# Kernel optimization log

Measured on AMD Instinct MI355X. Metric: run time of the kernel, lower is better.

## Reference

```python
import jax, jax.numpy as jnp
import numpy as np

H = 1024   # hidden size
NH = 16    # num attention heads
HD = H // NH  # head dim = 64


def setup_inputs() -> dict:
    key = jax.random.key(0)
    ks = jax.random.split(key, 8)
    B, S = 2, 2048
    scale = 0.02
    return {
        "hidden_states": jax.random.normal(ks[0], (B, S, H), dtype=jnp.float32),
        "attention_mask": jnp.zeros((B, 1, 1, S), dtype=jnp.float32),
        "Wq": jax.random.normal(ks[1], (H, H), dtype=jnp.float32) * scale,
        "bq": jnp.zeros((H,), dtype=jnp.float32),
        "Wk": jax.random.normal(ks[2], (H, H), dtype=jnp.float32) * scale,
        "bk": jnp.zeros((H,), dtype=jnp.float32),
        "Wv": jax.random.normal(ks[3], (H, H), dtype=jnp.float32) * scale,
        "bv": jnp.zeros((H,), dtype=jnp.float32),
    }


def reference(hidden_states, attention_mask, Wq, bq, Wk, bk, Wv, bv):
    B, S, _ = hidden_states.shape

    def split_heads(x):  # [B,S,H] -> [B,NH,S,HD]
        return x.reshape(B, S, NH, HD).transpose(0, 2, 1, 3)

    q = split_heads(hidden_states @ Wq.T + bq)
    k = split_heads(hidden_states @ Wk.T + bk)
    v = split_heads(hidden_states @ Wv.T + bv)

    # raw attention scores [B,NH,S,S]
    scores = jnp.einsum("bhqd,bhkd->bhqk", q, k) / jnp.sqrt(jnp.float32(HD))
    scores = scores + attention_mask  # additive mask, broadcast [B,1,1,S]
    probs = jax.nn.softmax(scores, axis=-1)
    # dropout(p=0.1) is identity in eval mode

    ctx = jnp.einsum("bhqk,bhkd->bhqd", probs, v)  # [B,NH,S,HD]
    return ctx.transpose(0, 2, 1, 3).reshape(B, S, H)
```

## Files before the change

### kernel.cpp

```cpp
#include <hip/hip_runtime.h>
#include <hip/hip_bf16.h>
#include <math.h>

#define HSZ 1024
#define NHD 16
#define SEQ 2048
#define BSZ 2
#define MTOT (BSZ*SEQ)

typedef __attribute__((ext_vector_type(4)))  float  f32x4;
typedef __attribute__((ext_vector_type(8)))  __bf16 bf16x8;

#define LOG2E 1.4426950408889634f

#if __has_builtin(__builtin_amdgcn_exp2f)
#define EXP2(x) __builtin_amdgcn_exp2f(x)
#else
#define EXP2(x) exp2f(x)
#endif

__device__ __forceinline__ unsigned short f2bf(float x) {
    union { float f; unsigned u; } v; v.f = x;
    unsigned r = v.u + 0x7FFFu + ((v.u >> 16) & 1u);
    return (unsigned short)(r >> 16);
}
__device__ __forceinline__ float bf2f(unsigned short u) {
    union { unsigned u; float f; } v; v.u = ((unsigned)u) << 16; return v.f;
}
__device__ __forceinline__ unsigned cvtpk(float lo, float hi) {
    unsigned r;
    asm("v_cvt_pk_bf16_f32 %0, %1, %2" : "=v"(r) : "v"(lo), "v"(hi));
    return r;
}

__global__ __launch_bounds__(256) void cvt_all(
    const float* __restrict__ h,  unsigned short* __restrict__ hd,
    const float* __restrict__ w0, unsigned short* __restrict__ w0d,
    const float* __restrict__ w1, unsigned short* __restrict__ w1d,
    const float* __restrict__ w2, unsigned short* __restrict__ w2d,
    const float* __restrict__ mask, unsigned short* __restrict__ mexpb)
{
    const int bid = blockIdx.x;
    if (bid >= 3584) {
        const int o = ((bid - 3584) * 256 + threadIdx.x) * 8;
        float4 a = *(const float4*)(mask + o);
        float4 b = *(const float4*)(mask + o + 4);
        uint4 v;
        v.x = f2bf(EXP2(a.x * LOG2E)) | ((unsigned)f2bf(EXP2(a.y * LOG2E)) << 16);
        v.y = f2bf(EXP2(a.z * LOG2E)) | ((unsigned)f2bf(EXP2(a.w * LOG2E)) << 16);
        v.z = f2bf(EXP2(b.x * LOG2E)) | ((unsigned)f2bf(EXP2(b.y * LOG2E)) << 16);
        v.w = f2bf(EXP2(b.z * LOG2E)) | ((unsigned)f2bf(EXP2(b.w * LOG2E)) << 16);
        *(uint4*)(mexpb + o) = v;
        return;
    }
    const float* s; unsigned short* d; int i;
    if (bid < 2048)      { s = h;  d = hd;  i = bid; }
    else if (bid < 2560) { s = w0; d = w0d; i = bid - 2048; }
    else if (bid < 3072) { s = w1; d = w1d; i = bid - 2560; }
    else                 { s = w2; d = w2d; i = bid - 3072; }
    const int o = (i * 256 + threadIdx.x) * 8;
    float4 a = *(const float4*)(s + o);
    float4 b = *(const float4*)(s + o + 4);
    uint4 v;
    v.x = f2bf(a.x) | ((unsigned)f2bf(a.y) << 16);
    v.y = f2bf(a.z) | ((unsigned)f2bf(a.w) << 16);
    v.z = f2bf(b.x) | ((unsigned)f2bf(b.y) << 16);
    v.w = f2bf(b.z) | ((unsigned)f2bf(b.w) << 16);
    *(uint4*)(d + o) = v;
}

__global__ __launch_bounds__(256) void qkv_gemm(
    const unsigned short* __restrict__ hb,
    const unsigned short* __restrict__ wq,
    const unsigned short* __restrict__ wk,
    const unsigned short* __restrict__ wv,
    const float* __restrict__ bq, const float* __restrict__ bk,
    const float* __restrict__ bv, const unsigned short* __restrict__ mexpb,
    unsigned short* __restrict__ qo, char* __restrict__ ko,
    char* __restrict__ vo)
{
    __shared__ __align__(16) unsigned short As[128 * 32];
    __shared__ __align__(16) unsigned short Bs[128 * 32];

    const int t = threadIdx.x;
    const int w = t >> 6, l = t & 63, g = l >> 4, c = l & 15;
    const int bn = blockIdx.x, bm = blockIdx.y;
    const int which = bn >> 3;
    const int n0 = (bn & 7) << 7;
    const int m0 = bm << 7;
    const unsigned short* W = (which == 0) ? wq : (which == 1) ? wk : wv;
    const float* bb = (which == 0) ? bq : (which == 1) ? bk : bv;
    const float scale = (which == 0) ? 0.125f * LOG2E : 1.0f;
    const int wr = w >> 1, wc = w & 1;

    float mexpf[16];
    if (which == 2) {
        #pragma unroll
        for (int mi = 0; mi < 4; ++mi) {
            const int mrow = m0 + wr * 64 + mi * 16 + g * 4;
            const int bi = mrow >> 11, si = mrow & 2047;
            const unsigned short* mp = mexpb + bi * SEQ + si;
            uint2 mv = *(const uint2*)mp;
            mexpf[mi * 4 + 0] = bf2f((unsigned short)(mv.x & 0xFFFF));
            mexpf[mi * 4 + 1] = bf2f((unsigned short)(mv.x >> 16));
            mexpf[mi * 4 + 2] = bf2f((unsigned short)(mv.y & 0xFFFF));
            mexpf[mi * 4 + 3] = bf2f((unsigned short)(mv.y >> 16));
        }
    }

    f32x4 acc[4][4];
    #pragma unroll
    for (int mi = 0; mi < 4; ++mi)
        #pragma unroll
        for (int ni = 0; ni < 4; ++ni) acc[mi][ni] = {0.f, 0.f, 0.f, 0.f};

    for (int k0 = 0; k0 < HSZ; k0 += 32) {
        #pragma unroll
        for (int i2 = 0; i2 < 2; ++i2) {
            const int chunk = 2 * w + i2;
            const int row = (chunk << 4) + (l >> 2);
            const int sg = (l & 3) ^ ((row >> 1) & 3);
            const char* ga = (const char*)hb +
                (((size_t)(m0 + row) << 10) + k0) * 2 + sg * 16;
            const char* gb = (const char*)W +
                (((size_t)(n0 + row) << 10) + k0) * 2 + sg * 16;
            __builtin_amdgcn_global_load_lds(
                (const __attribute__((address_space(1))) unsigned*)ga,
                (__attribute__((address_space(3))) unsigned*)((char*)As + chunk * 1024),
                16, 0, 0);
            __builtin_amdgcn_global_load_lds(
                (const __attribute__((address_space(1))) unsigned*)gb,
                (__attribute__((address_space(3))) unsigned*)((char*)Bs + chunk * 1024),
                16, 0, 0);
        }
        __syncthreads();

        bf16x8 af[4], bfr[4];
        #pragma unroll
        for (int mi = 0; mi < 4; ++mi) {
            const int row = wr * 64 + mi * 16 + c;
            const int gg = g ^ ((row >> 1) & 3);
            af[mi] = *(const bf16x8*)((const char*)As + row * 64 + gg * 16);
        }
        #pragma unroll
        for (int ni = 0; ni < 4; ++ni) {
            const int row = wc * 64 + ni * 16 + c;
            const int gg = g ^ ((row >> 1) & 3);
            bfr[ni] = *(const bf16x8*)((const char*)Bs + row * 64 + gg * 16);
        }
        #pragma unroll
        for (int mi = 0; mi < 4; ++mi)
            #pragma unroll
            for (int ni = 0; ni < 4; ++ni)
                acc[mi][ni] = __builtin_amdgcn_mfma_f32_16x16x32_bf16(
                    af[mi], bfr[ni], acc[mi][ni], 0, 0, 0);
        __syncthreads();
    }

    #pragma unroll
    for (int ni = 0; ni < 4; ++ni) {
        const int ncol = n0 + wc * 64 + ni * 16 + c;
        const int hh = ncol >> 6, d = ncol & 63;
        const float bsc = bb[ncol] * scale;
        #pragma unroll
        for (int mi = 0; mi < 4; ++mi) {
            #pragma unroll
            for (int j = 0; j < 4; ++j) {
                const int mrow = m0 + wr * 64 + mi * 16 + g * 4 + j;
                const int bi = mrow >> 11, si = mrow & 2047;
                float vf = acc[mi][ni][j] * scale + bsc;
                if (which == 2) vf *= mexpf[mi * 4 + j];
                const unsigned short val = f2bf(vf);
                const size_t bhoff = (size_t)(bi * NHD + hh);
                if (which == 0) {
                    qo[((bhoff * SEQ + si) << 6) + d] = val;
                } else if (which == 1) {
                    char* p = ko + (bhoff << 18) + ((size_t)(si >> 6) << 13)
                            + ((si & 63) << 7) + (((d << 1)) ^ ((si & 7) << 4));
                    *(unsigned short*)p = val;
                } else {
                    char* p = vo + (bhoff << 18) + ((size_t)(si >> 6) << 13)
                            + (d << 7) + (((si & 63) << 1) ^ ((d & 7) << 4));
                    *(unsigned short*)p = val;
                }
            }
        }
    }
}

__global__ __launch_bounds__(256) void attn_mfma(
    const unsigned short* __restrict__ qb, const char* __restrict__ kb,
    const char* __restrict__ vb, const unsigned short* __restrict__ mexpb,
    float* __restrict__ out)
{
    __shared__ __align__(16) char Kt[3][8192];
    __shared__ __align__(16) char Vt[3][8192];
    __shared__ __align__(16) unsigned Pl[4][16][32];

    const int t = threadIdx.x;
    const int w = t >> 6, l = t & 63, g = l >> 4, c = l & 15;
    const int qt = blockIdx.x, h = blockIdx.y, b = blockIdx.z;
    const int bh = b * NHD + h;
    const int q0 = qt * 128 + w * 32;

    const unsigned short* qp = qb + ((size_t)bh * SEQ + q0) * 64;
    const char* kbase = kb + ((size_t)bh << 18);
    const char* vbase = vb + ((size_t)bh << 18);
    const unsigned short* mep = mexpb + b * SEQ;

    bf16x8 qf[2][2];
    #pragma unroll
    for (int qh = 0; qh < 2; ++qh)
        #pragma unroll
        for (int p = 0; p < 2; ++p)
            qf[qh][p] = *(const bf16x8*)(qp + (qh * 16 + c) * 64 + p * 32 + g * 8);

    f32x4 o0[4], o1[4];
    #pragma unroll
    for (int tt = 0; tt < 4; ++tt) { o0[tt] = {0.f,0.f,0.f,0.f}; o1[tt] = {0.f,0.f,0.f,0.f}; }
    f32x4 ls0 = {0.f,0.f,0.f,0.f}, ls1 = {0.f,0.f,0.f,0.f};

    auto STAGE = [&](int tile, int buf) {
        const char* kg = kbase + tile * 8192 + w * 2048 + l * 16;
        const char* vg = vbase + tile * 8192 + w * 2048 + l * 16;
        #pragma unroll
        for (int i = 0; i < 2; ++i) {
            __builtin_amdgcn_global_load_lds(
                (const __attribute__((address_space(1))) unsigned*)(kg + i * 1024),
                (__attribute__((address_space(3))) unsigned*)(&Kt[buf][w * 2048 + i * 1024]),
                16, 0, 0);
            __builtin_amdgcn_global_load_lds(
                (const __attribute__((address_space(1))) unsigned*)(vg + i * 1024),
                (__attribute__((address_space(3))) unsigned*)(&Vt[buf][w * 2048 + i * 1024]),
                16, 0, 0);
        }
    };

    STAGE(0, 0);
    STAGE(1, 1);

    int cur = 0;
    for (int kt = 0; kt < 32; ++kt) {
        const int kv0 = kt * 64;

        if (kt >= 30) { asm volatile("s_waitcnt vmcnt(0)" ::: "memory"); }
        else          { asm volatile("s_waitcnt vmcnt(4)" ::: "memory"); }
        __builtin_amdgcn_s_barrier();
        __builtin_amdgcn_sched_barrier(0);

        if (kt < 30) {
            int slot = cur + 2; if (slot >= 3) slot -= 3;
            STAGE(kt + 2, slot);
        }

        bf16x8 mf[2];
        #pragma unroll
        for (int blk = 0; blk < 2; ++blk)
            mf[blk] = *(const bf16x8*)(mep + kv0 + blk * 32 + g * 8);

        f32x4 s0[4], s1[4];
        #pragma unroll
        for (int t2 = 0; t2 < 4; ++t2) { s0[t2] = {0.f,0.f,0.f,0.f}; s1[t2] = {0.f,0.f,0.f,0.f}; }
        __builtin_amdgcn_s_setprio(1);
        #pragma unroll
        for (int t2 = 0; t2 < 4; ++t2) {
            const bf16x8 k0 = *(const bf16x8*)(&Kt[cur][(t2 * 16 + c) * 128
                                 + ((g * 16) ^ ((c & 7) << 4))]);
            const bf16x8 k1 = *(const bf16x8*)(&Kt[cur][(t2 * 16 + c) * 128
                                 + ((64 + g * 16) ^ ((c & 7) << 4))]);
            s0[t2] = __builtin_amdgcn_mfma_f32_16x16x32_bf16(k0, qf[0][0], s0[t2], 0, 0, 0);
            s0[t2] = __builtin_amdgcn_mfma_f32_16x16x32_bf16(k1, qf[0][1], s0[t2], 0, 0, 0);
            s1[t2] = __builtin_amdgcn_mfma_f32_16x16x32_bf16(k0, qf[1][0], s1[t2], 0, 0, 0);
            s1[t2] = __builtin_amdgcn_mfma_f32_16x16x32_bf16(k1, qf[1][1], s1[t2], 0, 0, 0);
        }
        __builtin_amdgcn_s_setprio(0);

        bf16x8 vfr[4][2];
        #pragma unroll
        for (int tt = 0; tt < 4; ++tt)
            #pragma unroll
            for (int blk = 0; blk < 2; ++blk)
                vfr[tt][blk] = *(const bf16x8*)(&Vt[cur][(tt * 16 + c) * 128
                                     + ((blk * 64 + g * 16) ^ ((c & 7) << 4))]);

        #pragma unroll
        for (int t2 = 0; t2 < 4; ++t2) {
            s0[t2][0] = EXP2(s0[t2][0]); s0[t2][1] = EXP2(s0[t2][1]);
            s0[t2][2] = EXP2(s0[t2][2]); s0[t2][3] = EXP2(s0[t2][3]);
        }
        #pragma unroll
        for (int t2 = 0; t2 < 4; ++t2) {
            uint2 pr;
            pr.x = cvtpk(s0[t2][0], s0[t2][1]);
            pr.y = cvtpk(s0[t2][2], s0[t2][3]);
            *(uint2*)&Pl[w][c][(8 * t2 + 2 * g) ^ ((c & 7) << 2)] = pr;
        }
        {
            bf16x8 pfr[2];
            #pragma unroll
            for (int blk = 0; blk < 2; ++blk)
                pfr[blk] = *(const bf16x8*)&Pl[w][c][(16 * blk + 4 * g) ^ ((c & 7) << 2)];
            __builtin_amdgcn_s_setprio(1);
            #pragma unroll
            for (int blk = 0; blk < 2; ++blk)
                ls0 = __builtin_amdgcn_mfma_f32_16x16x32_bf16(mf[blk], pfr[blk], ls0, 0, 0, 0);
            #pragma unroll
            for (int tt = 0; tt < 4; ++tt)
                #pragma unroll
                for (int blk = 0; blk < 2; ++blk)
                    o0[tt] = __builtin_amdgcn_mfma_f32_16x16x32_bf16(vfr[tt][blk], pfr[blk], o0[tt], 0, 0, 0);
            __builtin_amdgcn_s_setprio(0);
        }

        #pragma unroll
        for (int t2 = 0; t2 < 4; ++t2) {
            s1[t2][0] = EXP2(s1[t2][0]); s1[t2][1] = EXP2(s1[t2][1]);
            s1[t2][2] = EXP2(s1[t2][2]); s1[t2][3] = EXP2(s1[t2][3]);
        }
        #pragma unroll
        for (int t2 = 0; t2 < 4; ++t2) {
            uint2 pr;
            pr.x = cvtpk(s1[t2][0], s1[t2][1]);
            pr.y = cvtpk(s1[t2][2], s1[t2][3]);
            *(uint2*)&Pl[w][c][(8 * t2 + 2 * g) ^ ((c & 7) << 2)] = pr;
        }
        {
            bf16x8 pfr[2];
            #pragma unroll
            for (int blk = 0; blk < 2; ++blk)
                pfr[blk] = *(const bf16x8*)&Pl[w][c][(16 * blk + 4 * g) ^ ((c & 7) << 2)];
            __builtin_amdgcn_s_setprio(1);
            #pragma unroll
            for (int blk = 0; blk < 2; ++blk)
                ls1 = __builtin_amdgcn_mfma_f32_16x16x32_bf16(mf[blk], pfr[blk], ls1, 0, 0, 0);
            #pragma unroll
            for (int tt = 0; tt < 4; ++tt)
                #pragma unroll
                for (int blk = 0; blk < 2; ++blk)
                    o1[tt] = __builtin_amdgcn_mfma_f32_16x16x32_bf16(vfr[tt][blk], pfr[blk], o1[tt], 0, 0, 0);
            __builtin_amdgcn_s_setprio(0);
        }

        ++cur; if (cur == 3) cur = 0;
    }

    const float li0 = 1.f / ls0[0];
    const float li1 = 1.f / ls1[0];
    #pragma unroll
    for (int tt = 0; tt < 4; ++tt) {
        const size_t r0 = ((size_t)(b * SEQ + q0 + c) << 10) + h * 64 + 16 * tt + 4 * g;
        out[r0 + 0] = o0[tt][0] * li0;
        out[r0 + 1] = o0[tt][1] * li0;
        out[r0 + 2] = o0[tt][2] * li0;
        out[r0 + 3] = o0[tt][3] * li0;
        const size_t r1 = ((size_t)(b * SEQ + q0 + 16 + c) << 10) + h * 64 + 16 * tt + 4 * g;
        out[r1 + 0] = o1[tt][0] * li1;
        out[r1 + 1] = o1[tt][1] * li1;
        out[r1 + 2] = o1[tt][2] * li1;
        out[r1 + 3] = o1[tt][3] * li1;
    }
}

extern "C" void kernel_launch(void* const* d_in, const int* in_sizes, int n_in,
                              void* d_out, int out_size, void* d_ws, size_t ws_size,
                              hipStream_t stream) {
    const float* hid  = (const float*)d_in[0];
    const float* mask = (const float*)d_in[1];
    const float* Wq   = (const float*)d_in[2];
    const float* bq   = (const float*)d_in[3];
    const float* Wk   = (const float*)d_in[4];
    const float* bk   = (const float*)d_in[5];
    const float* Wv   = (const float*)d_in[6];
    const float* bv   = (const float*)d_in[7];
    float* out = (float*)d_out;

    char* ws = (char*)d_ws;
    unsigned short* qbf = (unsigned short*)(ws);
    char*           kbf = ws + 8388608;
    char*           vbf = ws + 16777216;
    unsigned short* hbf = (unsigned short*)(ws + 25165824);
    unsigned short* wqb = (unsigned short*)(ws + 33554432);
    unsigned short* wkb = (unsigned short*)(ws + 35651584);
    unsigned short* wvb = (unsigned short*)(ws + 37748736);
    unsigned short* mxb = (unsigned short*)(ws + 39845888);

    cvt_all<<<3586, 256, 0, stream>>>(hid, hbf, Wq, wqb, Wk, wkb, Wv, wvb,
                                      mask, mxb);
    qkv_gemm<<<dim3(24, 32), 256, 0, stream>>>(hbf, wqb, wkb, wvb,
                                               bq, bk, bv, mxb, qbf, kbf, vbf);
    attn_mfma<<<dim3(16, NHD, BSZ), 256, 0, stream>>>(qbf, kbf, vbf, mxb, out);
}
```

Measured before the change: 115.6 us.

## Triple-buffer QKV GEMM LDS tiles with async prefetch two stages ahead

The QKV projection GEMM's shared-memory tiles become a three-slot ring buffer. Global-to-LDS loads for k-step kk+2 are issued before the MFMA work of step kk, with explicit vmcnt waits and a single barrier per iteration replacing the two __syncthreads. MFMA issue priority is also raised with s_setprio. This is meant to hide global load latency in the GEMM, at the cost of three times the LDS footprint, which may lower occupancy.

```diff
diff --git a/kernel.cpp b/kernel.cpp
--- a/kernel.cpp
+++ b/kernel.cpp
@@ -79,8 +79,8 @@
     unsigned short* __restrict__ qo, char* __restrict__ ko,
     char* __restrict__ vo)
 {
-    __shared__ __align__(16) unsigned short As[128 * 32];
-    __shared__ __align__(16) unsigned short Bs[128 * 32];
+    __shared__ __align__(16) unsigned short As[3][128 * 32];
+    __shared__ __align__(16) unsigned short Bs[3][128 * 32];
 
     const int t = threadIdx.x;
     const int w = t >> 6, l = t & 63, g = l >> 4, c = l & 15;
@@ -114,7 +114,8 @@
         #pragma unroll
         for (int ni = 0; ni < 4; ++ni) acc[mi][ni] = {0.f, 0.f, 0.f, 0.f};
 
-    for (int k0 = 0; k0 < HSZ; k0 += 32) {
+    auto STAGE = [&](int kidx, int buf) {
+        const int k0 = kidx * 32;
         #pragma unroll
         for (int i2 = 0; i2 < 2; ++i2) {
             const int chunk = 2 * w + i2;
@@ -126,35 +127,53 @@
                 (((size_t)(n0 + row) << 10) + k0) * 2 + sg * 16;
             __builtin_amdgcn_global_load_lds(
                 (const __attribute__((address_space(1))) unsigned*)ga,
-                (__attribute__((address_space(3))) unsigned*)((char*)As + chunk * 1024),
+                (__attribute__((address_space(3))) unsigned*)((char*)As[buf] + chunk * 1024),
                 16, 0, 0);
             __builtin_amdgcn_global_load_lds(
                 (const __attribute__((address_space(1))) unsigned*)gb,
-                (__attribute__((address_space(3))) unsigned*)((char*)Bs + chunk * 1024),
+                (__attribute__((address_space(3))) unsigned*)((char*)Bs[buf] + chunk * 1024),
                 16, 0, 0);
         }
-        __syncthreads();
+    };
+
+    STAGE(0, 0);
+    STAGE(1, 1);
+
+    int cur = 0;
+    for (int kk = 0; kk < 32; ++kk) {
+        if (kk >= 30) { asm volatile("s_waitcnt vmcnt(0)" ::: "memory"); }
+        else          { asm volatile("s_waitcnt vmcnt(4)" ::: "memory"); }
+        __builtin_amdgcn_s_barrier();
+        __builtin_amdgcn_sched_barrier(0);
+
+        if (kk < 30) {
+            int slot = cur + 2; if (slot >= 3) slot -= 3;
+            STAGE(kk + 2, slot);
+        }
 
         bf16x8 af[4], bfr[4];
         #pragma unroll
         for (int mi = 0; mi < 4; ++mi) {
             const int row = wr * 64 + mi * 16 + c;
             const int gg = g ^ ((row >> 1) & 3);
-            af[mi] = *(const bf16x8*)((const char*)As + row * 64 + gg * 16);
+            af[mi] = *(const bf16x8*)((const char*)As[cur] + row * 64 + gg * 16);
         }
         #pragma unroll
         for (int ni = 0; ni < 4; ++ni) {
             const int row = wc * 64 + ni * 16 + c;
             const int gg = g ^ ((row >> 1) & 3);
-            bfr[ni] = *(const bf16x8*)((const char*)Bs + row * 64 + gg * 16);
-        }
+            bfr[ni] = *(const bf16x8*)((const char*)Bs[cur] + row * 64 + gg * 16);
+        }
+        __builtin_amdgcn_s_setprio(1);
         #pragma unroll
         for (int mi = 0; mi < 4; ++mi)
             #pragma unroll
             for (int ni = 0; ni < 4; ++ni)
                 acc[mi][ni] = __builtin_amdgcn_mfma_f32_16x16x32_bf16(
                     af[mi], bfr[ni], acc[mi][ni], 0, 0, 0);
-        __syncthreads();
+        __builtin_amdgcn_s_setprio(0);
+
+        ++cur; if (cur == 3) cur = 0;
     }
 
     #pragma unroll
```

Result: slower. 118.4 us (+2.4%).
